# Kernel optimization log

Hardware: AMD Instinct MI355X
Metric: run time of the kernel (lower is better)

The kernel has to match this reference:

```python
import jax, jax.numpy as jnp
import numpy as np

N = 50000      # nodes
F = 128        # in_channels
H = 4          # heads
C = 32         # out_channels per head
E = 800000     # edges (before self-loops)
NEG_SLOPE = 0.2


def setup_inputs() -> dict:
    key = jax.random.key(0)
    ks = jax.random.split(key, 10)
    x = jax.random.normal(ks[0], (N, F), dtype=jnp.float32)
    edge_index = jax.random.randint(ks[1], (2, E), 0, N, dtype=jnp.int32)
    s = 1.0 / np.sqrt(F)
    Wl = jax.random.uniform(ks[2], (H * C, F), jnp.float32, -s, s)
    bl = jax.random.uniform(ks[3], (H * C,), jnp.float32, -s, s)
    Wr = jax.random.uniform(ks[4], (H * C, F), jnp.float32, -s, s)
    br = jax.random.uniform(ks[5], (H * C,), jnp.float32, -s, s)
    Ws = jax.random.uniform(ks[6], (H * C, F), jnp.float32, -s, s)
    bs = jax.random.uniform(ks[7], (H * C,), jnp.float32, -s, s)
    att = jax.random.normal(ks[8], (H, C), jnp.float32) * (1.0 / np.sqrt(C))
    bias = jnp.zeros((H * C,), jnp.float32)
    return {"x": x, "edge_index": edge_index, "Wl": Wl, "bl": bl,
            "Wr": Wr, "br": br, "Ws": Ws, "bs": bs, "att": att, "bias": bias}


def reference(x, edge_index, Wl, bl, Wr, br, Ws, bs, att, bias):
    # add self loops (add_self_loops=True, edge_dim=None)
    loop = jnp.arange(N, dtype=edge_index.dtype)
    src = jnp.concatenate([edge_index[0], loop])  # j (source / neighbor)
    dst = jnp.concatenate([edge_index[1], loop])  # i (target, softmax segment)

    xl = (x @ Wl.T + bl).reshape(N, H, C)  # attention source transform (lin_l = lin_lAP)
    xr = (x @ Wr.T + br).reshape(N, H, C)  # attention target transform (lin_r = lin_rAP)
    xs = (x @ Ws.T + bs).reshape(N, H, C)  # aggregation transform (lin_s, linAggrSharing=False)

    # GATv2 edge score: a^T LeakyReLU(Theta_l x_j + Theta_r x_i)
    e = jax.nn.leaky_relu(xl[src] + xr[dst], NEG_SLOPE)      # [E+N, H, C]
    score = jnp.einsum('ehc,hc->eh', e, att)                 # [E+N, H]

    # segment softmax over incoming edges of each target node
    m = jax.ops.segment_max(score, dst, num_segments=N)      # [N, H]
    p = jnp.exp(score - m[dst])
    denom = jax.ops.segment_sum(p, dst, num_segments=N)      # [N, H]
    alpha = p / denom[dst]                                   # [E+N, H]

    # weighted scatter-add aggregation of lin_s-transformed sources
    out = jax.ops.segment_sum(xs[src] * alpha[..., None], dst, num_segments=N)
    return out.reshape(N, H * C) + bias                      # concat=True
```

## Files before the change

kernel.cpp:

```cpp
#include <hip/hip_runtime.h>
#include <hip/hip_bf16.h>

#define GN 50000
#define GF 128
#define GH 4
#define GC 32
#define GE 800000
#define GETOT (GE + GN)
#define HC 128
#define NEG 0.2f

#define TBLK 391
#define TTOT (TBLK * 3)
#define SBLK ((GETOT + 255) / 256)

typedef __bf16 bf16x8 __attribute__((ext_vector_type(8)));
typedef float  f32x4  __attribute__((ext_vector_type(4)));
typedef unsigned short ushort8 __attribute__((ext_vector_type(8)));

__device__ __forceinline__ ushort f32_to_bf16_rne(float f) {
    unsigned u = __float_as_uint(f);
    return (ushort)((u + 0x7fffu + ((u >> 16) & 1u)) >> 16);
}

__device__ __forceinline__ bf16x8 cvt8(const float* p) {
    float4 v0 = *(const float4*)p;
    float4 v1 = *(const float4*)(p + 4);
    ushort8 o;
    o[0] = f32_to_bf16_rne(v0.x); o[1] = f32_to_bf16_rne(v0.y);
    o[2] = f32_to_bf16_rne(v0.z); o[3] = f32_to_bf16_rne(v0.w);
    o[4] = f32_to_bf16_rne(v1.x); o[5] = f32_to_bf16_rne(v1.y);
    o[6] = f32_to_bf16_rne(v1.z); o[7] = f32_to_bf16_rne(v1.w);
    return __builtin_bit_cast(bf16x8, o);
}

__global__ __launch_bounds__(256) void conv_w(
    const float* __restrict__ Wl, const float* __restrict__ Wr,
    const float* __restrict__ Ws, ushort* __restrict__ Wb,
    int* __restrict__ deg)
{
    int idx = blockIdx.x * 256 + threadIdx.x;
    if (idx < 3 * GF * GF / 8) {
        int m = idx / 2048;
        int e = (idx - m * 2048) * 8;
        const float* W = (m == 0) ? Wl : (m == 1) ? Wr : Ws;
        float4 v0 = *(const float4*)&W[e];
        float4 v1 = *(const float4*)&W[e + 4];
        ushort8 o;
        o[0] = f32_to_bf16_rne(v0.x); o[1] = f32_to_bf16_rne(v0.y);
        o[2] = f32_to_bf16_rne(v0.z); o[3] = f32_to_bf16_rne(v0.w);
        o[4] = f32_to_bf16_rne(v1.x); o[5] = f32_to_bf16_rne(v1.y);
        o[6] = f32_to_bf16_rne(v1.z); o[7] = f32_to_bf16_rne(v1.w);
        *(ushort8*)&Wb[m * 16384 + e] = o;
    }
    int z = idx - 6144;
    if (z >= 0 && z < GN / 4)
        *(int4*)&deg[z * 4] = make_int4(0, 0, 0, 0);
}

__global__ __launch_bounds__(256) void fused_transform_slot(
    const float* __restrict__ x, const ushort* __restrict__ Wb,
    const float* __restrict__ bl, const float* __restrict__ br,
    const float* __restrict__ bs,
    const int* __restrict__ ei, int* __restrict__ deg, int* __restrict__ slot,
    ushort* __restrict__ xi, float* __restrict__ xr)
{
    if (blockIdx.x < SBLK) {
        int e = blockIdx.x * 256 + threadIdx.x;
        if (e < GETOT) {
            int dst = (e < GE) ? ei[GE + e] : (e - GE);
            slot[e] = atomicAdd(&deg[dst], 1);
        }
        return;
    }

    const int tb    = blockIdx.x - SBLK;
    const int m     = tb / TBLK;
    const int bx    = tb - m * TBLK;
    const int wave  = threadIdx.x >> 6;
    const int lane  = threadIdx.x & 63;
    const int colb  = lane & 15;
    const int klane = lane >> 4;
    const int row0  = bx * 128 + wave * 32;

    bf16x8 a[2][4];
#pragma unroll
    for (int s = 0; s < 2; ++s) {
        int rA = row0 + s * 16 + colb;
        const float* ap = x + (size_t)min(rA, GN - 1) * GF + klane * 8;
#pragma unroll
        for (int kb = 0; kb < 4; ++kb)
            a[s][kb] = cvt8(ap + kb * 32);
    }

    const ushort* wb = Wb + m * 16384 + colb * GF + klane * 8;

    f32x4 acc[2][8];
#pragma unroll
    for (int s = 0; s < 2; ++s)
#pragma unroll
        for (int n = 0; n < 8; ++n) acc[s][n] = (f32x4){0.f, 0.f, 0.f, 0.f};

#pragma unroll
    for (int kb = 0; kb < 4; ++kb) {
        bf16x8 b[8];
#pragma unroll
        for (int n = 0; n < 8; ++n)
            b[n] = *(const bf16x8*)(wb + n * 2048 + kb * 32);
#pragma unroll
        for (int n = 0; n < 8; ++n) {
            acc[0][n] = __builtin_amdgcn_mfma_f32_16x16x32_bf16(a[0][kb], b[n], acc[0][n], 0, 0, 0);
            acc[1][n] = __builtin_amdgcn_mfma_f32_16x16x32_bf16(a[1][kb], b[n], acc[1][n], 0, 0, 0);
        }
    }

    const float* bia = (m == 0) ? bl : (m == 1) ? br : bs;
    const int moff = (m == 2) ? 2 : 0;
#pragma unroll
    for (int s = 0; s < 2; ++s) {
        int rD0 = row0 + s * 16 + klane * 4;
#pragma unroll
        for (int n = 0; n < 8; ++n) {
            int col = n * 16 + colb;
            float bv = bia[col];
#pragma unroll
            for (int r = 0; r < 4; ++r) {
                int row = rD0 + r;
                if (row < GN) {
                    float v = acc[s][n][r] + bv;
                    if (m == 1)
                        xr[(size_t)row * HC + col] = v;
                    else
                        xi[(size_t)row * 256 + (col >> 1) * 4 + (col & 1) + moff]
                            = f32_to_bf16_rne(v);
                }
            }
        }
    }
}

__global__ __launch_bounds__(1024) void scan_kernel(const int* __restrict__ deg,
                                                    int* __restrict__ rowstart)
{
    __shared__ int sums[1024];
    const int t = threadIdx.x;
    const int CH = 52;
    const int start = t * CH;
    const int end = min(start + CH, GN);

    int s = 0;
    if (start + CH <= GN) {
#pragma unroll
        for (int g = 0; g < 13; ++g) {
            int4 v = *(const int4*)&deg[start + g * 4];
            s += v.x + v.y + v.z + v.w;
        }
    } else {
        for (int i = start; i < end; ++i) s += deg[i];
    }
    sums[t] = s;
    __syncthreads();
    for (int off = 1; off < 1024; off <<= 1) {
        int v = (t >= off) ? sums[t - off] : 0;
        __syncthreads();
        sums[t] += v;
        __syncthreads();
    }
    int run = sums[t] - s;
    if (start + CH <= GN) {
#pragma unroll
        for (int g = 0; g < 13; ++g) {
            int4 v = *(const int4*)&deg[start + g * 4];
            int4 w;
            w.x = run;
            w.y = run + v.x;
            w.z = run + v.x + v.y;
            w.w = run + v.x + v.y + v.z;
            run += v.x + v.y + v.z + v.w;
            *(int4*)&rowstart[start + g * 4] = w;
        }
    } else {
        for (int i = start; i < end; ++i) { rowstart[i] = run; run += deg[i]; }
    }
    if (t == 1023) rowstart[GN] = run;
}

__global__ void scatter_kernel(const int* __restrict__ ei,
                               const int* __restrict__ rowstart,
                               const int* __restrict__ slot,
                               int* __restrict__ csr_src)
{
    int e = blockIdx.x * 256 + threadIdx.x;
    if (e >= GETOT) return;
    int src, dst;
    if (e < GE) { src = ei[e]; dst = ei[GE + e]; }
    else        { src = dst = e - GE; }
    csr_src[rowstart[dst] + slot[e]] = src;
}

__device__ __forceinline__ void edge_acc(uint2 xv, float2 xr2, float2 at2,
                                         bool live, float& denom,
                                         float& ax, float& ay)
{
    float zx = __uint_as_float((xv.x & 0xffffu) << 16) + xr2.x;
    float zy = __uint_as_float(xv.x & 0xffff0000u) + xr2.y;
    zx = (zx > 0.f) ? zx : NEG * zx;
    zy = (zy > 0.f) ? zy : NEG * zy;
    float sc = fmaf(zx, at2.x, zy * at2.y);
    sc += __shfl_xor(sc, 1, 64);
    sc += __shfl_xor(sc, 2, 64);
    sc += __shfl_xor(sc, 4, 64);
    sc += __shfl_xor(sc, 8, 64);
    float pe = live ? __expf(sc) : 0.f;
    denom += pe;
    ax = fmaf(pe, __uint_as_float((xv.y & 0xffffu) << 16), ax);
    ay = fmaf(pe, __uint_as_float(xv.y & 0xffff0000u), ay);
}

__global__ __launch_bounds__(256) void gat_kernel(
    const ushort* __restrict__ xi, const float* __restrict__ xr,
    const float* __restrict__ att, const float* __restrict__ bias,
    const int* __restrict__ rowstart, const int* __restrict__ csr_src,
    float* __restrict__ out)
{
    const int wave = threadIdx.x >> 6;
    const int lane = threadIdx.x & 63;
    const int node = blockIdx.x * 4 + wave;
    const int l4 = lane * 4;

    const float2 xr2 = *(const float2*)&xr[(size_t)node * HC + lane * 2];
    const float2 at2 = *(const float2*)&att[lane * 2];
    const float2 bi2 = *(const float2*)&bias[lane * 2];

    const int s0 = rowstart[node];
    const int s1 = rowstart[node + 1];

    float denom = 0.f, ax = 0.f, ay = 0.f;
    for (int base = s0; base < s1; base += 64) {
        int nsrc = (base + lane < s1) ? csr_src[base + lane] : 0;
        int cnt = min(64, s1 - base);
        for (int t = 0; t < cnt; t += 4) {
            int sA = __shfl(nsrc, t, 64);
            int sB = __shfl(nsrc, t + 1, 64);
            int sC = __shfl(nsrc, t + 2, 64);
            int sD = __shfl(nsrc, t + 3, 64);
            uint2 vA = *(const uint2*)&xi[(size_t)sA * 256 + l4];
            uint2 vB = *(const uint2*)&xi[(size_t)sB * 256 + l4];
            uint2 vC = *(const uint2*)&xi[(size_t)sC * 256 + l4];
            uint2 vD = *(const uint2*)&xi[(size_t)sD * 256 + l4];
            edge_acc(vA, xr2, at2, true,          denom, ax, ay);
            edge_acc(vB, xr2, at2, (t + 1 < cnt), denom, ax, ay);
            edge_acc(vC, xr2, at2, (t + 2 < cnt), denom, ax, ay);
            edge_acc(vD, xr2, at2, (t + 3 < cnt), denom, ax, ay);
        }
    }
    const float inv = 1.f / denom;
    float2 o;
    o.x = fmaf(ax, inv, bi2.x);
    o.y = fmaf(ay, inv, bi2.y);
    *(float2*)&out[(size_t)node * HC + lane * 2] = o;
}

extern "C" void kernel_launch(void* const* d_in, const int* in_sizes, int n_in,
                              void* d_out, int out_size, void* d_ws, size_t ws_size,
                              hipStream_t stream)
{
    const float* x   = (const float*)d_in[0];
    const int*   ei  = (const int*)  d_in[1];
    const float* Wl  = (const float*)d_in[2];
    const float* bl  = (const float*)d_in[3];
    const float* Wr  = (const float*)d_in[4];
    const float* br  = (const float*)d_in[5];
    const float* Ws  = (const float*)d_in[6];
    const float* bs  = (const float*)d_in[7];
    const float* att = (const float*)d_in[8];
    const float* bias= (const float*)d_in[9];
    float* out = (float*)d_out;

    ushort* xi = (ushort*)d_ws;
    ushort* Wb = xi + (size_t)GN * 256;
    float*  xr = (float*)(Wb + 3 * GF * GF);
    int* deg      = (int*)(xr + (size_t)GN * HC);
    int* rowstart = deg + GN;
    int* slot     = rowstart + GN + 1;
    int* csr_src  = slot + GETOT;

    conv_w<<<(6144 + GN / 4 + 255) / 256, 256, 0, stream>>>(Wl, Wr, Ws, Wb, deg);

    fused_transform_slot<<<SBLK + TTOT, 256, 0, stream>>>(
        x, Wb, bl, br, bs, ei, deg, slot, xi, xr);

    scan_kernel<<<1, 1024, 0, stream>>>(deg, rowstart);

    scatter_kernel<<<SBLK, 256, 0, stream>>>(ei, rowstart, slot, csr_src);

    gat_kernel<<<GN / 4, 256, 0, stream>>>((const ushort*)xi, xr, att, bias,
                                           rowstart, csr_src, out);
}
```

Baseline: 274.3 us.

## Reuse converted x tile across three projections and use DPP for score reduction

The transform kernel now gives each block 64 rows and loops over all three weight matrices, so each x tile is loaded and converted to bf16 once instead of three times. This cuts global reads of x and the conversion work, but each block does more serial work and the grid shrinks, which may reduce parallelism. Separately, the 16-lane score reduction in the edge loop swaps `__shfl_xor` for DPP quad_perm and row_ror adds. These avoid LDS-based cross-lane traffic on the hot aggregation path.

```diff
diff --git a/kernel.cpp b/kernel.cpp
--- a/kernel.cpp
+++ b/kernel.cpp
@@ -10,8 +10,7 @@
 #define HC 128
 #define NEG 0.2f
 
-#define TBLK 391
-#define TTOT (TBLK * 3)
+#define TBLK ((GN + 63) / 64)
 #define SBLK ((GETOT + 255) / 256)
 
 typedef __bf16 bf16x8 __attribute__((ext_vector_type(8)));
@@ -32,6 +31,13 @@
     o[4] = f32_to_bf16_rne(v1.x); o[5] = f32_to_bf16_rne(v1.y);
     o[6] = f32_to_bf16_rne(v1.z); o[7] = f32_to_bf16_rne(v1.w);
     return __builtin_bit_cast(bf16x8, o);
+}
+
+template<int CTRL>
+__device__ __forceinline__ float dpp_add(float v) {
+    int s = __builtin_bit_cast(int, v);
+    int y = __builtin_amdgcn_update_dpp(s, s, CTRL, 0xF, 0xF, false);
+    return v + __builtin_bit_cast(float, y);
 }
 
 __global__ __launch_bounds__(256) void conv_w(
@@ -74,51 +80,43 @@
         return;
     }
 
-    const int tb    = blockIdx.x - SBLK;
-    const int m     = tb / TBLK;
-    const int bx    = tb - m * TBLK;
+    const int bx    = blockIdx.x - SBLK;
     const int wave  = threadIdx.x >> 6;
     const int lane  = threadIdx.x & 63;
     const int colb  = lane & 15;
     const int klane = lane >> 4;
-    const int row0  = bx * 128 + wave * 32;
-
-    bf16x8 a[2][4];
-#pragma unroll
-    for (int s = 0; s < 2; ++s) {
-        int rA = row0 + s * 16 + colb;
+    const int row0  = bx * 64 + wave * 16;
+
+    bf16x8 a[4];
+    {
+        int rA = row0 + colb;
         const float* ap = x + (size_t)min(rA, GN - 1) * GF + klane * 8;
 #pragma unroll
         for (int kb = 0; kb < 4; ++kb)
-            a[s][kb] = cvt8(ap + kb * 32);
-    }
-
-    const ushort* wb = Wb + m * 16384 + colb * GF + klane * 8;
-
-    f32x4 acc[2][8];
-#pragma unroll
-    for (int s = 0; s < 2; ++s)
-#pragma unroll
-        for (int n = 0; n < 8; ++n) acc[s][n] = (f32x4){0.f, 0.f, 0.f, 0.f};
-
-#pragma unroll
-    for (int kb = 0; kb < 4; ++kb) {
-        bf16x8 b[8];
-#pragma unroll
-        for (int n = 0; n < 8; ++n)
-            b[n] = *(const bf16x8*)(wb + n * 2048 + kb * 32);
-#pragma unroll
-        for (int n = 0; n < 8; ++n) {
-            acc[0][n] = __builtin_amdgcn_mfma_f32_16x16x32_bf16(a[0][kb], b[n], acc[0][n], 0, 0, 0);
-            acc[1][n] = __builtin_amdgcn_mfma_f32_16x16x32_bf16(a[1][kb], b[n], acc[1][n], 0, 0, 0);
-        }
-    }
-
-    const float* bia = (m == 0) ? bl : (m == 1) ? br : bs;
-    const int moff = (m == 2) ? 2 : 0;
-#pragma unroll
-    for (int s = 0; s < 2; ++s) {
-        int rD0 = row0 + s * 16 + klane * 4;
+            a[kb] = cvt8(ap + kb * 32);
+    }
+
+    for (int m = 0; m < 3; ++m) {
+        const ushort* wb = Wb + m * 16384 + colb * GF + klane * 8;
+
+        f32x4 acc[8];
+#pragma unroll
+        for (int n = 0; n < 8; ++n) acc[n] = (f32x4){0.f, 0.f, 0.f, 0.f};
+
+#pragma unroll
+        for (int kb = 0; kb < 4; ++kb) {
+            bf16x8 b[8];
+#pragma unroll
+            for (int n = 0; n < 8; ++n)
+                b[n] = *(const bf16x8*)(wb + n * 2048 + kb * 32);
+#pragma unroll
+            for (int n = 0; n < 8; ++n)
+                acc[n] = __builtin_amdgcn_mfma_f32_16x16x32_bf16(a[kb], b[n], acc[n], 0, 0, 0);
+        }
+
+        const float* bia = (m == 0) ? bl : (m == 1) ? br : bs;
+        const int moff = (m == 2) ? 2 : 0;
+        const int rD0 = row0 + klane * 4;
 #pragma unroll
         for (int n = 0; n < 8; ++n) {
             int col = n * 16 + colb;
@@ -127,7 +125,7 @@
             for (int r = 0; r < 4; ++r) {
                 int row = rD0 + r;
                 if (row < GN) {
-                    float v = acc[s][n][r] + bv;
+                    float v = acc[n][r] + bv;
                     if (m == 1)
                         xr[(size_t)row * HC + col] = v;
                     else
@@ -207,10 +205,10 @@
     zx = (zx > 0.f) ? zx : NEG * zx;
     zy = (zy > 0.f) ? zy : NEG * zy;
     float sc = fmaf(zx, at2.x, zy * at2.y);
-    sc += __shfl_xor(sc, 1, 64);
-    sc += __shfl_xor(sc, 2, 64);
-    sc += __shfl_xor(sc, 4, 64);
-    sc += __shfl_xor(sc, 8, 64);
+    sc = dpp_add<0xB1>(sc);
+    sc = dpp_add<0x4E>(sc);
+    sc = dpp_add<0x124>(sc);
+    sc = dpp_add<0x128>(sc);
     float pe = live ? __expf(sc) : 0.f;
     denom += pe;
     ax = fmaf(pe, __uint_as_float((xv.y & 0xffffu) << 16), ax);
@@ -287,7 +285,7 @@
 
     conv_w<<<(6144 + GN / 4 + 255) / 256, 256, 0, stream>>>(Wl, Wr, Ws, Wb, deg);
 
-    fused_transform_slot<<<SBLK + TTOT, 256, 0, stream>>>(
+    fused_transform_slot<<<SBLK + TBLK, 256, 0, stream>>>(
         x, Wb, bl, br, bs, ei, deg, slot, xi, xr);
 
     scan_kernel<<<1, 1024, 0, stream>>>(deg, rowstart);
```

Result: slower. 285.9 us (+4.2%).
